# Kernel tuning notes

Measured on AMD Instinct MI355X. Metric: run time of the kernel, lower is better.

## Reference

```python
import jax, jax.numpy as jnp
import numpy as np

N0, N1, E, T = 100000, 20000, 320000, 8
D_IN, H, E_IN, C = 128, 64, 15, 16
F_LSTM = E_IN + 1  # edge feats + appended time channel


def lstm_last(x, lengths, Wih, Whh, b):
    """Unidirectional LSTM; returns hidden state at step lengths-1 per row.
    x: [E, T, F]; lengths: [E] int (1..T)."""
    Eb, Tn, _ = x.shape
    Hh = Whh.shape[0]
    xt = jnp.swapaxes(x, 0, 1)  # [T, E, F]
    h0 = jnp.zeros((Eb, Hh), x.dtype)

    def step(carry, inp):
        h, c, last_h = carry
        x_t, t = inp
        gates = x_t @ Wih + h @ Whh + b  # [E, 4H]
        i, f, g, o = jnp.split(gates, 4, axis=-1)
        c = jax.nn.sigmoid(f) * c + jax.nn.sigmoid(i) * jnp.tanh(g)
        h = jax.nn.sigmoid(o) * jnp.tanh(c)
        valid = (t < lengths)[:, None]
        last_h = jnp.where(valid, h, last_h)
        return (h, c, last_h), None

    (_, _, last_h), _ = jax.lax.scan(step, (h0, h0, h0), (xt, jnp.arange(Tn)))
    return last_h


def setup_inputs() -> dict:
    key = jax.random.key(0)
    ks = jax.random.split(key, 20)
    inp = {
        "node_features": jax.random.normal(ks[0], (N0, D_IN), jnp.float32),
        "edge_features": jax.random.normal(ks[1], (E, T, E_IN), jnp.float32),
        "seq_times": jax.random.uniform(ks[2], (E, T), jnp.float32),
        "subg_norm": jax.random.uniform(ks[3], (N1, 1), jnp.float32),
        "node_p_w": jax.random.normal(ks[4], (D_IN, 1), jnp.float32) * 0.01,
        "lstm_Wih": jax.random.normal(ks[5], (F_LSTM, 4 * H), jnp.float32) / np.sqrt(F_LSTM),
        "lstm_Whh": jax.random.normal(ks[6], (H, 4 * H), jnp.float32) / np.sqrt(H),
        "lstm_b": jnp.zeros((4 * H,), jnp.float32),
        "edge_out_W": jax.random.normal(ks[7], (D_IN + H, H), jnp.float32) / np.sqrt(D_IN + H),
        "edge_out_b": jnp.zeros((H,), jnp.float32),
        "node_W": jax.random.normal(ks[8], (D_IN + H, H), jnp.float32) / np.sqrt(D_IN + H),
        "node_b": jnp.zeros((H,), jnp.float32),
        "fc_W": jax.random.normal(ks[9], (H, C), jnp.float32) / np.sqrt(H),
        "fc_b": jnp.zeros((C,), jnp.float32),
        "edge_len": jax.random.randint(ks[10], (E,), 1, T + 1, jnp.int32),
        "src": jax.random.randint(ks[11], (E,), 0, N0, jnp.int32),
        "dst": jax.random.randint(ks[12], (E,), 0, N1, jnp.int32),
        "layer_nid": jax.random.randint(ks[13], (N1,), 0, N0, jnp.int32),
    }
    return inp


def reference(node_features, edge_features, seq_times, subg_norm, node_p_w,
              lstm_Wih, lstm_Whh, lstm_b, edge_out_W, edge_out_b,
              node_W, node_b, fc_W, fc_b,
              edge_len, src, dst, layer_nid):
    n1 = layer_nid.shape[0]
    # self features for destination nodes
    self_h = node_features[layer_nid]                         # [N1, D_IN]
    self_h_tmp = jnp.concatenate(
        [self_h, jnp.zeros((n1, H), self_h.dtype)], axis=1) @ edge_out_W + edge_out_b
    # message: gather src h, ragged LSTM over edge sequences, low-rank removal
    h_src = node_features[src]                                # [E, D_IN]
    e = jnp.concatenate([edge_features, seq_times[..., None]], axis=-1)  # [E,T,F]
    e_enc = lstm_last(e, edge_len, lstm_Wih, lstm_Whh, lstm_b)           # [E, H]
    h_proj = h_src - (h_src @ node_p_w) @ node_p_w.T          # rank-1 removal
    m = jax.nn.relu(jnp.concatenate([h_proj, e_enc], axis=1) @ edge_out_W + edge_out_b)
    # reduce: scatter-sum into destination nodes
    agg = jax.ops.segment_sum(m, dst, num_segments=n1)        # [N1, H]
    # NodeUpdate
    hu = (agg - self_h_tmp) * subg_norm
    act = jax.nn.relu(jnp.concatenate([self_h, hu], axis=1) @ node_W + node_b)
    return act @ fc_W + fc_b                                  # [N1, C]
```

## Files before the change

### kernel.cpp

```cpp
#include <hip/hip_runtime.h>

#define N0c 100000
#define N1c 20000
#define Ec 320000
#define NBLK ((Ec + 1023) / 1024)

typedef _Float16 f16;
typedef _Float16 f16x2 __attribute__((ext_vector_type(2)));

#define LOG2E 1.442695040888963f

__device__ __forceinline__ float tanh_(float x) {
    return 2.f * __builtin_amdgcn_rcpf(1.f + __builtin_amdgcn_exp2f(-2.f * LOG2E * x)) - 1.f;
}
__device__ __forceinline__ float dot2(uint w, uint v, float acc) {
#if __has_builtin(__builtin_amdgcn_fdot2)
    return __builtin_amdgcn_fdot2(__builtin_bit_cast(f16x2, w),
                                  __builtin_bit_cast(f16x2, v), acc, false);
#else
    f16x2 a = __builtin_bit_cast(f16x2, w);
    f16x2 b = __builtin_bit_cast(f16x2, v);
    return acc + (float)a[0] * (float)b[0] + (float)a[1] * (float)b[1];
#endif
}
__device__ __forceinline__ uint packh(float a, float b) {
    f16x2 p;
    p[0] = (f16)a;
    p[1] = (f16)b;
    return __builtin_bit_cast(uint, p);
}

__global__ void count_kernel(const int* __restrict__ elen, int* __restrict__ bc) {
    __shared__ int h[8];
    if (threadIdx.x < 8) h[threadIdx.x] = 0;
    __syncthreads();
    const int base = blockIdx.x * 1024;
    for (int i = threadIdx.x; i < 1024; i += 256) {
        int e = base + i;
        if (e < Ec) atomicAdd(&h[elen[e] - 1], 1);
    }
    __syncthreads();
    if (threadIdx.x < 8) bc[blockIdx.x * 8 + threadIdx.x] = h[threadIdx.x];
}

__global__ void offs_kernel(const int* __restrict__ bc, int* __restrict__ bo) {
    __shared__ int s[NBLK * 8];
    __shared__ int base[8];
    const int tid = threadIdx.x;
    for (int i = tid; i < NBLK * 8; i += 256) s[i] = bc[i];
    __syncthreads();
    if (tid == 0) {
        int tot[8];
        for (int b = 0; b < 8; ++b) {
            int t = 0;
            for (int blk = 0; blk < NBLK; ++blk) t += s[blk * 8 + b];
            tot[b] = t;
        }
        int run = 0;
        for (int b = 0; b < 8; ++b) { base[b] = run; run += tot[b]; }
    }
    __syncthreads();
    if (tid < 8) {
        int run = base[tid];
        for (int blk = 0; blk < NBLK; ++blk) {
            int t = s[blk * 8 + tid];
            s[blk * 8 + tid] = run;
            run += t;
        }
    }
    __syncthreads();
    for (int i = tid; i < NBLK * 8; i += 256) bo[i] = s[i];
}

__global__ void scatter2_kernel(const int* __restrict__ elen, const int* __restrict__ bo,
                                int* __restrict__ lperm, int* __restrict__ lenq) {
    __shared__ int cnt[256][9];
    const int tid = threadIdx.x;
    const int base = blockIdx.x * 1024 + tid * 4;
    int lens[4];
    int lc0 = 0, lc1 = 0, lc2 = 0, lc3 = 0, lc4 = 0, lc5 = 0, lc6 = 0, lc7 = 0;
    #pragma unroll
    for (int j = 0; j < 4; ++j) {
        int e = base + j;
        int l = (e < Ec) ? elen[e] - 1 : -1;
        lens[j] = l;
        lc0 += (l == 0); lc1 += (l == 1); lc2 += (l == 2); lc3 += (l == 3);
        lc4 += (l == 4); lc5 += (l == 5); lc6 += (l == 6); lc7 += (l == 7);
    }
    cnt[tid][0] = lc0; cnt[tid][1] = lc1; cnt[tid][2] = lc2; cnt[tid][3] = lc3;
    cnt[tid][4] = lc4; cnt[tid][5] = lc5; cnt[tid][6] = lc6; cnt[tid][7] = lc7;
    __syncthreads();
    if (tid < 8) {
        int run = bo[blockIdx.x * 8 + tid];
        for (int i = 0; i < 256; ++i) {
            int t = cnt[i][tid];
            cnt[i][tid] = run;
            run += t;
        }
    }
    __syncthreads();
    #pragma unroll
    for (int b = 0; b < 8; ++b) {
        int p = cnt[tid][b];
        #pragma unroll
        for (int j = 0; j < 4; ++j) {
            if (lens[j] == b) { lperm[p] = base + j; lenq[p] = b + 1; ++p; }
        }
    }
}

__global__ void dhist_kernel(const int* __restrict__ dst, int* __restrict__ hist) {
    int e = blockIdx.x * blockDim.x + threadIdx.x;
    if (e < Ec) atomicAdd(&hist[dst[e]], 1);
}

__global__ void dscan_kernel(int* __restrict__ hist) {
    __shared__ int s[N1c];
    __shared__ int psum[256];
    const int tid = threadIdx.x;
    const int CH = (N1c + 255) / 256;
    for (int i = tid; i < N1c; i += 256) s[i] = hist[i];
    __syncthreads();
    int loc = 0;
    #pragma unroll 1
    for (int j = 0; j < CH; ++j) {
        int i = tid * CH + j;
        if (i < N1c) loc += s[i];
    }
    psum[tid] = loc;
    __syncthreads();
    if (tid == 0) {
        int run = 0;
        for (int t = 0; t < 256; ++t) { int v = psum[t]; psum[t] = run; run += v; }
    }
    __syncthreads();
    int run = psum[tid];
    #pragma unroll 1
    for (int j = 0; j < CH; ++j) {
        int i = tid * CH + j;
        if (i < N1c) { int v = s[i]; s[i] = run; run += v; }
    }
    __syncthreads();
    for (int i = tid; i < N1c; i += 256) hist[i] = s[i];
}

__global__ void dscatter_kernel(const int* __restrict__ dst, int* __restrict__ cursor,
                                int* __restrict__ perm) {
    int e = blockIdx.x * blockDim.x + threadIdx.x;
    if (e < Ec) {
        int pos = atomicAdd(&cursor[dst[e]], 1);
        perm[pos] = e;
    }
}

__global__ void wprep_kernel(const float* __restrict__ Whh, const float* __restrict__ Wih,
                             const float* __restrict__ eW,
                             uint* __restrict__ wpk, uint* __restrict__ ewc) {
    int idx = blockIdx.x * 256 + threadIdx.x;
    if (idx < 40 * 256) {
        int r4 = idx >> 8, l = (idx >> 2) & 63, i = idx & 3;
        float s = (i == 2) ? (-2.f * LOG2E) : (-LOG2E);
        uint v;
        if (r4 < 32)
            v = packh(s * Whh[(2 * r4) * 256 + i * 64 + l],
                      s * Whh[(2 * r4 + 1) * 256 + i * 64 + l]);
        else {
            int kp = r4 - 32;
            v = packh(s * Wih[(2 * kp) * 256 + i * 64 + l],
                      s * Wih[(2 * kp + 1) * 256 + i * 64 + l]);
        }
        wpk[idx] = v;
    }
    if (idx < 24 * 256) {
        int c4 = idx >> 8, l = (idx >> 2) & 63, i = idx & 3;
        int cp = c4 * 4 + i;
        ewc[idx] = packh(eW[(2 * cp) * 64 + l], eW[(2 * cp + 1) * 64 + l]);
    }
}

__global__ void xprep_kernel(const float* __restrict__ ef, const float* __restrict__ st,
                             const int* __restrict__ lperm, uint* __restrict__ Xpk) {
    int idx = blockIdx.x * 256 + threadIdx.x;
    int i = idx >> 3, t = idx & 7;
    int e = lperm[i];
    float v[16];
    #pragma unroll
    for (int f = 0; f < 15; ++f) v[f] = ef[(size_t)e * 120 + t * 15 + f];
    v[15] = st[(size_t)e * 8 + t];
    uint* dst = Xpk + (size_t)idx * 8;
    #pragma unroll
    for (int j = 0; j < 8; ++j) dst[j] = packh(v[2 * j], v[2 * j + 1]);
}


__global__ __launch_bounds__(256)
void lstm4_kernel(const uint4* __restrict__ wpk4, const float* __restrict__ lb,
                  const uint* __restrict__ Xpk, const int* __restrict__ lperm,
                  const int* __restrict__ lenq, f16* __restrict__ hb)
{
    __shared__ __align__(16) uint4 sW[2560];
    __shared__ __align__(16) f16 sH[4][4 * 64];

    const int tid = threadIdx.x;
    #pragma unroll
    for (int i = 0; i < 10; ++i) sW[i * 256 + tid] = wpk4[i * 256 + tid];
    __syncthreads();

    const int lane = tid & 63;
    const int wv = tid >> 6;

    const float b0 = -LOG2E * lb[lane];
    const float b1 = -LOG2E * lb[64 + lane];
    const float b2 = -2.f * LOG2E * lb[128 + lane];
    const float b3 = -LOG2E * lb[192 + lane];
    f16* myH = sH[wv];
    const uint4* wl = sW + lane;

    const int nT = Ec / 4;
    for (int tile = blockIdx.x * 4 + wv; tile < nT; tile += gridDim.x * 4) {
        const int p0 = tile * 4;
        const int oe0 = lperm[p0], oe1 = lperm[p0 + 1], oe2 = lperm[p0 + 2], oe3 = lperm[p0 + 3];
        const int l0 = lenq[p0], l1 = lenq[p0 + 1], l2 = lenq[p0 + 2], l3 = lenq[p0 + 3];
        const int tmax = max(max(l0, l1), max(l2, l3));

        const uint* xr = Xpk + (size_t)p0 * 64;

        float hA = 0.f, cA = 0.f, hB = 0.f, cB = 0.f;
        float hC = 0.f, cC = 0.f, hD = 0.f, cD = 0.f;

        for (int t = 0; t < tmax; ++t) {
            float a0A = b0, a1A = b1, a2A = b2, a3A = b3;
            float a0B = b0, a1B = b1, a2B = b2, a3B = b3;
            float a0C = b0, a1C = b1, a2C = b2, a3C = b3;
            float a0D = b0, a1D = b1, a2D = b2, a3D = b3;

            if (t > 0) {
                #pragma unroll
                for (int jb = 0; jb < 8; ++jb) {
                    uint4 hA4 = *(const uint4*)(myH + 0 * 64 + jb * 8);
                    uint4 hB4 = *(const uint4*)(myH + 1 * 64 + jb * 8);
                    uint4 hC4 = *(const uint4*)(myH + 2 * 64 + jb * 8);
                    uint4 hD4 = *(const uint4*)(myH + 3 * 64 + jb * 8);
                    #pragma unroll
                    for (int i = 0; i < 4; ++i) {
                        uint4 w = wl[(jb * 4 + i) * 64];
                        uint hpA = (i == 0) ? hA4.x : (i == 1) ? hA4.y : (i == 2) ? hA4.z : hA4.w;
                        uint hpB = (i == 0) ? hB4.x : (i == 1) ? hB4.y : (i == 2) ? hB4.z : hB4.w;
                        uint hpC = (i == 0) ? hC4.x : (i == 1) ? hC4.y : (i == 2) ? hC4.z : hC4.w;
                        uint hpD = (i == 0) ? hD4.x : (i == 1) ? hD4.y : (i == 2) ? hD4.z : hD4.w;
                        a0A = dot2(w.x, hpA, a0A); a1A = dot2(w.y, hpA, a1A);
                        a2A = dot2(w.z, hpA, a2A); a3A = dot2(w.w, hpA, a3A);
                        a0B = dot2(w.x, hpB, a0B); a1B = dot2(w.y, hpB, a1B);
                        a2B = dot2(w.z, hpB, a2B); a3B = dot2(w.w, hpB, a3B);
                        a0C = dot2(w.x, hpC, a0C); a1C = dot2(w.y, hpC, a1C);
                        a2C = dot2(w.z, hpC, a2C); a3C = dot2(w.w, hpC, a3C);
                        a0D = dot2(w.x, hpD, a0D); a1D = dot2(w.y, hpD, a1D);
                        a2D = dot2(w.z, hpD, a2D); a3D = dot2(w.w, hpD, a3D);
                    }
                }
            }

            #pragma unroll
            for (int k4 = 0; k4 < 8; ++k4) {
                uint4 w = wl[(32 + k4) * 64];
                uint xA = xr[t * 8 + k4];
                uint xB = xr[64 + t * 8 + k4];
                uint xC = xr[128 + t * 8 + k4];
                uint xD = xr[192 + t * 8 + k4];
                a0A = dot2(w.x, xA, a0A); a1A = dot2(w.y, xA, a1A);
                a2A = dot2(w.z, xA, a2A); a3A = dot2(w.w, xA, a3A);
                a0B = dot2(w.x, xB, a0B); a1B = dot2(w.y, xB, a1B);
                a2B = dot2(w.z, xB, a2B); a3B = dot2(w.w, xB, a3B);
                a0C = dot2(w.x, xC, a0C); a1C = dot2(w.y, xC, a1C);
                a2C = dot2(w.z, xC, a2C); a3C = dot2(w.w, xC, a3C);
                a0D = dot2(w.x, xD, a0D); a1D = dot2(w.y, xD, a1D);
                a2D = dot2(w.z, xD, a2D); a3D = dot2(w.w, xD, a3D);
            }

            {
                float ig = __builtin_amdgcn_rcpf(1.f + __builtin_amdgcn_exp2f(a0A));
                float fg = __builtin_amdgcn_rcpf(1.f + __builtin_amdgcn_exp2f(a1A));
                float gg = 2.f * __builtin_amdgcn_rcpf(1.f + __builtin_amdgcn_exp2f(a2A)) - 1.f;
                float og = __builtin_amdgcn_rcpf(1.f + __builtin_amdgcn_exp2f(a3A));
                float cn = fg * cA + ig * gg, hn = og * tanh_(cn);
                if (t < l0) { cA = cn; hA = hn; }
                ig = __builtin_amdgcn_rcpf(1.f + __builtin_amdgcn_exp2f(a0B));
                fg = __builtin_amdgcn_rcpf(1.f + __builtin_amdgcn_exp2f(a1B));
                gg = 2.f * __builtin_amdgcn_rcpf(1.f + __builtin_amdgcn_exp2f(a2B)) - 1.f;
                og = __builtin_amdgcn_rcpf(1.f + __builtin_amdgcn_exp2f(a3B));
                cn = fg * cB + ig * gg; hn = og * tanh_(cn);
                if (t < l1) { cB = cn; hB = hn; }
                ig = __builtin_amdgcn_rcpf(1.f + __builtin_amdgcn_exp2f(a0C));
                fg = __builtin_amdgcn_rcpf(1.f + __builtin_amdgcn_exp2f(a1C));
                gg = 2.f * __builtin_amdgcn_rcpf(1.f + __builtin_amdgcn_exp2f(a2C)) - 1.f;
                og = __builtin_amdgcn_rcpf(1.f + __builtin_amdgcn_exp2f(a3C));
                cn = fg * cC + ig * gg; hn = og * tanh_(cn);
                if (t < l2) { cC = cn; hC = hn; }
                ig = __builtin_amdgcn_rcpf(1.f + __builtin_amdgcn_exp2f(a0D));
                fg = __builtin_amdgcn_rcpf(1.f + __builtin_amdgcn_exp2f(a1D));
                gg = 2.f * __builtin_amdgcn_rcpf(1.f + __builtin_amdgcn_exp2f(a2D)) - 1.f;
                og = __builtin_amdgcn_rcpf(1.f + __builtin_amdgcn_exp2f(a3D));
                cn = fg * cD + ig * gg; hn = og * tanh_(cn);
                if (t < l3) { cD = cn; hD = hn; }
            }
            if (t + 1 < tmax) {
                myH[0 * 64 + lane] = (f16)hA;
                myH[1 * 64 + lane] = (f16)hB;
                myH[2 * 64 + lane] = (f16)hC;
                myH[3 * 64 + lane] = (f16)hD;
            }
        }

        hb[(size_t)oe0 * 64 + lane] = (f16)hA;
        hb[(size_t)oe1 * 64 + lane] = (f16)hB;
        hb[(size_t)oe2 * 64 + lane] = (f16)hC;
        hb[(size_t)oe3 * 64 + lane] = (f16)hD;
    }
}

__global__ __launch_bounds__(256, 2)
void mlp_kernel(const float* __restrict__ nf, const float* __restrict__ pw,
                const uint4* __restrict__ ewc4, const float* __restrict__ ebias,
                const int* __restrict__ src, const f16* __restrict__ hb,
                f16* __restrict__ mbuf)
{
    __shared__ __align__(16) f16 sCat[4][192];
    const int lane = threadIdx.x & 63;
    const int wv = threadIdx.x >> 6;

    uint ew[24][4];
    #pragma unroll
    for (int i = 0; i < 24; ++i) {
        uint4 v = ewc4[i * 64 + lane];
        ew[i][0] = v.x; ew[i][1] = v.y; ew[i][2] = v.z; ew[i][3] = v.w;
    }
    const float pwl = pw[lane], pwh = pw[64 + lane];
    const float ebl = ebias[lane];

    f16* myCat = sCat[wv];
    const int wid = blockIdx.x * 4 + wv;
    const int stride = gridDim.x * 4;
    for (int e = wid; e < Ec; e += stride) {
        const int s = src[e];
        float hs0 = nf[(size_t)s * 128 + lane];
        float hs1 = nf[(size_t)s * 128 + 64 + lane];
        float part = hs0 * pwl + hs1 * pwh;
        #pragma unroll
        for (int off = 32; off; off >>= 1) part += __shfl_xor(part, off);
        float he = (float)hb[(size_t)e * 64 + lane];
        myCat[lane] = (f16)(hs0 - part * pwl);
        myCat[64 + lane] = (f16)(hs1 - part * pwh);
        myCat[128 + lane] = (f16)he;
        const uint4* cp = (const uint4*)myCat;
        float m0 = 0.f, m1 = 0.f, m2 = 0.f, m3 = 0.f;
        #pragma unroll
        for (int i = 0; i < 24; ++i) {
            uint4 q = cp[i];
            m0 = dot2(ew[i][0], q.x, m0);
            m1 = dot2(ew[i][1], q.y, m1);
            m2 = dot2(ew[i][2], q.z, m2);
            m3 = dot2(ew[i][3], q.w, m3);
        }
        float m = fmaxf(m0 + m1 + m2 + m3 + ebl, 0.f);
        mbuf[(size_t)e * 64 + lane] = (f16)m;
    }
}

#define NB_WAVES 8
#define NB_THREADS (NB_WAVES * 64)
__global__ __launch_bounds__(NB_THREADS, 1)
void node_kernel(const float* __restrict__ nf,
                 const float* __restrict__ sgn,
                 const float* __restrict__ eW,
                 const float* __restrict__ ebias,
                 const float* __restrict__ nW,
                 const float* __restrict__ nbias,
                 const float* __restrict__ fcW,
                 const float* __restrict__ fcb,
                 const int* __restrict__ lnid,
                 const int* __restrict__ hist,
                 const int* __restrict__ perm,
                 const f16* __restrict__ m,
                 float* __restrict__ out,
                 int nWavesTotal)
{
    __shared__ float sEW[128 * 64];
    __shared__ float sNW[192 * 64];
    __shared__ float sFC[64 * 16];
    __shared__ float sCat[NB_WAVES][192];
    __shared__ float sAct[NB_WAVES][64];

    const int tid = threadIdx.x;
    for (int idx = tid; idx < 128 * 64; idx += NB_THREADS) sEW[idx] = eW[idx];
    for (int idx = tid; idx < 192 * 64; idx += NB_THREADS) sNW[idx] = nW[idx];
    for (int idx = tid; idx < 64 * 16; idx += NB_THREADS) sFC[idx] = fcW[idx];
    __syncthreads();

    const int lane = tid & 63;
    const int wv = tid >> 6;
    const int gwave = blockIdx.x * NB_WAVES + wv;

    const float ebv = ebias[lane];
    const float nbv = nbias[lane];
    const float fcbv = (lane < 16) ? fcb[lane] : 0.f;

    for (int n = gwave; n < N1c; n += nWavesTotal) {
        const int nid = lnid[n];
        float sh0 = nf[(size_t)nid * 128 + lane];
        float sh1 = nf[(size_t)nid * 128 + 64 + lane];
        sCat[wv][lane] = sh0;
        sCat[wv][64 + lane] = sh1;

        float tmp = ebv;
        #pragma unroll 8
        for (int cc = 0; cc < 128; ++cc) tmp += sCat[wv][cc] * sEW[cc * 64 + lane];

        const int o0 = (n == 0) ? 0 : hist[n - 1];
        const int o1 = hist[n];
        float av = 0.f;
        for (int base = o0; base < o1; base += 64) {
            int cnt = min(64, o1 - base);
            int pk = (lane < cnt) ? perm[base + lane] : 0;
            for (int j = 0; j < cnt; ++j) {
                int pe = __shfl(pk, j);
                av += (float)m[(size_t)pe * 64 + lane];
            }
        }

        float hu = (av - tmp) * sgn[n];
        sCat[wv][128 + lane] = hu;

        float acc = nbv;
        #pragma unroll 8
        for (int cc = 0; cc < 192; ++cc) acc += sCat[wv][cc] * sNW[cc * 64 + lane];
        acc = fmaxf(acc, 0.f);
        sAct[wv][lane] = acc;

        if (lane < 16) {
            float o = fcbv;
            #pragma unroll
            for (int j = 0; j < 64; ++j) o += sAct[wv][j] * sFC[j * 16 + lane];
            out[(size_t)n * 16 + lane] = o;
        }
    }
}

extern "C" void kernel_launch(void* const* d_in, const int* in_sizes, int n_in,
                              void* d_out, int out_size, void* d_ws, size_t ws_size,
                              hipStream_t stream) {
    const float* nf  = (const float*)d_in[0];
    const float* ef  = (const float*)d_in[1];
    const float* st  = (const float*)d_in[2];
    const float* sgn = (const float*)d_in[3];
    const float* pw  = (const float*)d_in[4];
    const float* Wih = (const float*)d_in[5];
    const float* Whh = (const float*)d_in[6];
    const float* lb  = (const float*)d_in[7];
    const float* eW  = (const float*)d_in[8];
    const float* eb  = (const float*)d_in[9];
    const float* nW  = (const float*)d_in[10];
    const float* nb  = (const float*)d_in[11];
    const float* fcW = (const float*)d_in[12];
    const float* fcb = (const float*)d_in[13];
    const int* elen = (const int*)d_in[14];
    const int* src  = (const int*)d_in[15];
    const int* dst  = (const int*)d_in[16];
    const int* lnid = (const int*)d_in[17];

    float* out = (float*)d_out;

    char* base = (char*)d_ws;
    int*  hist  = (int*) (base + 0);
    int*  dperm = (int*) (base + 81920);
    int*  bc    = (int*) (base + 1392640);
    int*  bo    = (int*) (base + 1409024);
    int*  lperm = (int*) (base + 1425408);
    int*  lenq  = (int*) (base + 2736128);
    uint* wpk   = (uint*)(base + 4046848);
    uint* ewc   = (uint*)(base + 4112384);
    uint* Xpk   = (uint*)(base + 4145152);
    f16*  hb    = (f16*) (base + 86065152);
    f16*  mbuf  = (f16*) (base + 127025152);

    hipMemsetAsync(hist, 0, 81920, stream);

    count_kernel<<<NBLK, 256, 0, stream>>>(elen, bc);
    offs_kernel<<<1, 256, 0, stream>>>(bc, bo);
    scatter2_kernel<<<NBLK, 256, 0, stream>>>(elen, bo, lperm, lenq);

    dhist_kernel<<<1250, 256, 0, stream>>>(dst, hist);
    dscan_kernel<<<1, 256, 0, stream>>>(hist);
    dscatter_kernel<<<1250, 256, 0, stream>>>(dst, hist, dperm);

    wprep_kernel<<<40, 256, 0, stream>>>(Whh, Wih, eW, wpk, ewc);
    xprep_kernel<<<10000, 256, 0, stream>>>(ef, st, lperm, Xpk);

    lstm4_kernel<<<2048, 256, 0, stream>>>((const uint4*)wpk, lb, Xpk, lperm, lenq, hb);

    mlp_kernel<<<1024, 256, 0, stream>>>(nf, pw, (const uint4*)ewc, eb, src, hb, mbuf);

    node_kernel<<<512, NB_THREADS, 0, stream>>>(
        nf, sgn, eW, eb, nW, nb, fcW, fcb, lnid, hist, dperm, mbuf, out,
        512 * NB_WAVES);
}
```

Measured before the change: 866.8 us.

## Process eight edge sequences per wave in LSTM kernel with 512-thread blocks

Each wave now runs the LSTM recurrence for eight edges at once instead of four. Every LDS weight load is reused across twice as many dot products, and blocks grow to 512 threads so the shared weight copy is amortised over more waves. The cost is higher register pressure from 32 accumulators plus eight h/c pairs, which may lower occupancy. Grouping eight length-sorted edges may also add some padding work where lengths differ within a tile.

```diff
diff --git a/kernel.cpp b/kernel.cpp
--- a/kernel.cpp
+++ b/kernel.cpp
@@ -193,17 +193,17 @@
 }
 
 
-__global__ __launch_bounds__(256)
-void lstm4_kernel(const uint4* __restrict__ wpk4, const float* __restrict__ lb,
+__global__ __launch_bounds__(512)
+void lstm8_kernel(const uint4* __restrict__ wpk4, const float* __restrict__ lb,
                   const uint* __restrict__ Xpk, const int* __restrict__ lperm,
                   const int* __restrict__ lenq, f16* __restrict__ hb)
 {
     __shared__ __align__(16) uint4 sW[2560];
-    __shared__ __align__(16) f16 sH[4][4 * 64];
+    __shared__ __align__(16) f16 sH[8][8 * 64];
 
     const int tid = threadIdx.x;
     #pragma unroll
-    for (int i = 0; i < 10; ++i) sW[i * 256 + tid] = wpk4[i * 256 + tid];
+    for (int i = 0; i < 5; ++i) sW[i * 512 + tid] = wpk4[i * 512 + tid];
     __syncthreads();
 
     const int lane = tid & 63;
@@ -216,46 +216,46 @@
     f16* myH = sH[wv];
     const uint4* wl = sW + lane;
 
-    const int nT = Ec / 4;
-    for (int tile = blockIdx.x * 4 + wv; tile < nT; tile += gridDim.x * 4) {
-        const int p0 = tile * 4;
-        const int oe0 = lperm[p0], oe1 = lperm[p0 + 1], oe2 = lperm[p0 + 2], oe3 = lperm[p0 + 3];
-        const int l0 = lenq[p0], l1 = lenq[p0 + 1], l2 = lenq[p0 + 2], l3 = lenq[p0 + 3];
-        const int tmax = max(max(l0, l1), max(l2, l3));
+    const int nT = Ec / 8;
+    for (int tile = blockIdx.x * 8 + wv; tile < nT; tile += gridDim.x * 8) {
+        const int p0 = tile * 8;
+        int oe[8], ln[8];
+        #pragma unroll
+        for (int j = 0; j < 8; ++j) { oe[j] = lperm[p0 + j]; ln[j] = lenq[p0 + j]; }
+        int tmax = ln[0];
+        #pragma unroll
+        for (int j = 1; j < 8; ++j) tmax = max(tmax, ln[j]);
 
         const uint* xr = Xpk + (size_t)p0 * 64;
 
-        float hA = 0.f, cA = 0.f, hB = 0.f, cB = 0.f;
-        float hC = 0.f, cC = 0.f, hD = 0.f, cD = 0.f;
+        float h8[8], c8[8];
+        #pragma unroll
+        for (int j = 0; j < 8; ++j) { h8[j] = 0.f; c8[j] = 0.f; }
 
         for (int t = 0; t < tmax; ++t) {
-            float a0A = b0, a1A = b1, a2A = b2, a3A = b3;
-            float a0B = b0, a1B = b1, a2B = b2, a3B = b3;
-            float a0C = b0, a1C = b1, a2C = b2, a3C = b3;
-            float a0D = b0, a1D = b1, a2D = b2, a3D = b3;
+            float a0[8], a1[8], a2[8], a3[8];
+            #pragma unroll
+            for (int j = 0; j < 8; ++j) { a0[j] = b0; a1[j] = b1; a2[j] = b2; a3[j] = b3; }
 
             if (t > 0) {
                 #pragma unroll
                 for (int jb = 0; jb < 8; ++jb) {
-                    uint4 hA4 = *(const uint4*)(myH + 0 * 64 + jb * 8);
-                    uint4 hB4 = *(const uint4*)(myH + 1 * 64 + jb * 8);
-                    uint4 hC4 = *(const uint4*)(myH + 2 * 64 + jb * 8);
-                    uint4 hD4 = *(const uint4*)(myH + 3 * 64 + jb * 8);
+                    uint4 hq[8];
+                    #pragma unroll
+                    for (int j = 0; j < 8; ++j)
+                        hq[j] = *(const uint4*)(myH + j * 64 + jb * 8);
                     #pragma unroll
                     for (int i = 0; i < 4; ++i) {
                         uint4 w = wl[(jb * 4 + i) * 64];
-                        uint hpA = (i == 0) ? hA4.x : (i == 1) ? hA4.y : (i == 2) ? hA4.z : hA4.w;
-                        uint hpB = (i == 0) ? hB4.x : (i == 1) ? hB4.y : (i == 2) ? hB4.z : hB4.w;
-                        uint hpC = (i == 0) ? hC4.x : (i == 1) ? hC4.y : (i == 2) ? hC4.z : hC4.w;
-                        uint hpD = (i == 0) ? hD4.x : (i == 1) ? hD4.y : (i == 2) ? hD4.z : hD4.w;
-                        a0A = dot2(w.x, hpA, a0A); a1A = dot2(w.y, hpA, a1A);
-                        a2A = dot2(w.z, hpA, a2A); a3A = dot2(w.w, hpA, a3A);
-                        a0B = dot2(w.x, hpB, a0B); a1B = dot2(w.y, hpB, a1B);
-                        a2B = dot2(w.z, hpB, a2B); a3B = dot2(w.w, hpB, a3B);
-                        a0C = dot2(w.x, hpC, a0C); a1C = dot2(w.y, hpC, a1C);
-                        a2C = dot2(w.z, hpC, a2C); a3C = dot2(w.w, hpC, a3C);
-                        a0D = dot2(w.x, hpD, a0D); a1D = dot2(w.y, hpD, a1D);
-                        a2D = dot2(w.z, hpD, a2D); a3D = dot2(w.w, hpD, a3D);
+                        #pragma unroll
+                        for (int j = 0; j < 8; ++j) {
+                            uint hp = (i == 0) ? hq[j].x : (i == 1) ? hq[j].y
+                                    : (i == 2) ? hq[j].z : hq[j].w;
+                            a0[j] = dot2(w.x, hp, a0[j]);
+                            a1[j] = dot2(w.y, hp, a1[j]);
+                            a2[j] = dot2(w.z, hp, a2[j]);
+                            a3[j] = dot2(w.w, hp, a3[j]);
+                        }
                     }
                 }
             }
@@ -263,58 +263,35 @@
             #pragma unroll
             for (int k4 = 0; k4 < 8; ++k4) {
                 uint4 w = wl[(32 + k4) * 64];
-                uint xA = xr[t * 8 + k4];
-                uint xB = xr[64 + t * 8 + k4];
-                uint xC = xr[128 + t * 8 + k4];
-                uint xD = xr[192 + t * 8 + k4];
-                a0A = dot2(w.x, xA, a0A); a1A = dot2(w.y, xA, a1A);
-                a2A = dot2(w.z, xA, a2A); a3A = dot2(w.w, xA, a3A);
-                a0B = dot2(w.x, xB, a0B); a1B = dot2(w.y, xB, a1B);
-                a2B = dot2(w.z, xB, a2B); a3B = dot2(w.w, xB, a3B);
-                a0C = dot2(w.x, xC, a0C); a1C = dot2(w.y, xC, a1C);
-                a2C = dot2(w.z, xC, a2C); a3C = dot2(w.w, xC, a3C);
-                a0D = dot2(w.x, xD, a0D); a1D = dot2(w.y, xD, a1D);
-                a2D = dot2(w.z, xD, a2D); a3D = dot2(w.w, xD, a3D);
+                #pragma unroll
+                for (int j = 0; j < 8; ++j) {
+                    uint xv = xr[j * 64 + t * 8 + k4];
+                    a0[j] = dot2(w.x, xv, a0[j]);
+                    a1[j] = dot2(w.y, xv, a1[j]);
+                    a2[j] = dot2(w.z, xv, a2[j]);
+                    a3[j] = dot2(w.w, xv, a3[j]);
+                }
             }
 
-            {
-                float ig = __builtin_amdgcn_rcpf(1.f + __builtin_amdgcn_exp2f(a0A));
-                float fg = __builtin_amdgcn_rcpf(1.f + __builtin_amdgcn_exp2f(a1A));
-                float gg = 2.f * __builtin_amdgcn_rcpf(1.f + __builtin_amdgcn_exp2f(a2A)) - 1.f;
-                float og = __builtin_amdgcn_rcpf(1.f + __builtin_amdgcn_exp2f(a3A));
-                float cn = fg * cA + ig * gg, hn = og * tanh_(cn);
-                if (t < l0) { cA = cn; hA = hn; }
-                ig = __builtin_amdgcn_rcpf(1.f + __builtin_amdgcn_exp2f(a0B));
-                fg = __builtin_amdgcn_rcpf(1.f + __builtin_amdgcn_exp2f(a1B));
-                gg = 2.f * __builtin_amdgcn_rcpf(1.f + __builtin_amdgcn_exp2f(a2B)) - 1.f;
-                og = __builtin_amdgcn_rcpf(1.f + __builtin_amdgcn_exp2f(a3B));
-                cn = fg * cB + ig * gg; hn = og * tanh_(cn);
-                if (t < l1) { cB = cn; hB = hn; }
-                ig = __builtin_amdgcn_rcpf(1.f + __builtin_amdgcn_exp2f(a0C));
-                fg = __builtin_amdgcn_rcpf(1.f + __builtin_amdgcn_exp2f(a1C));
-                gg = 2.f * __builtin_amdgcn_rcpf(1.f + __builtin_amdgcn_exp2f(a2C)) - 1.f;
-                og = __builtin_amdgcn_rcpf(1.f + __builtin_amdgcn_exp2f(a3C));
-                cn = fg * cC + ig * gg; hn = og * tanh_(cn);
-                if (t < l2) { cC = cn; hC = hn; }
-                ig = __builtin_amdgcn_rcpf(1.f + __builtin_amdgcn_exp2f(a0D));
-                fg = __builtin_amdgcn_rcpf(1.f + __builtin_amdgcn_exp2f(a1D));
-                gg = 2.f * __builtin_amdgcn_rcpf(1.f + __builtin_amdgcn_exp2f(a2D)) - 1.f;
-                og = __builtin_amdgcn_rcpf(1.f + __builtin_amdgcn_exp2f(a3D));
-                cn = fg * cD + ig * gg; hn = og * tanh_(cn);
-                if (t < l3) { cD = cn; hD = hn; }
+            #pragma unroll
+            for (int j = 0; j < 8; ++j) {
+                float ig = __builtin_amdgcn_rcpf(1.f + __builtin_amdgcn_exp2f(a0[j]));
+                float fg = __builtin_amdgcn_rcpf(1.f + __builtin_amdgcn_exp2f(a1[j]));
+                float gg = 2.f * __builtin_amdgcn_rcpf(1.f + __builtin_amdgcn_exp2f(a2[j])) - 1.f;
+                float og = __builtin_amdgcn_rcpf(1.f + __builtin_amdgcn_exp2f(a3[j]));
+                float cn = fg * c8[j] + ig * gg;
+                float hn = og * tanh_(cn);
+                if (t < ln[j]) { c8[j] = cn; h8[j] = hn; }
             }
             if (t + 1 < tmax) {
-                myH[0 * 64 + lane] = (f16)hA;
-                myH[1 * 64 + lane] = (f16)hB;
-                myH[2 * 64 + lane] = (f16)hC;
-                myH[3 * 64 + lane] = (f16)hD;
+                #pragma unroll
+                for (int j = 0; j < 8; ++j) myH[j * 64 + lane] = (f16)h8[j];
             }
         }
 
-        hb[(size_t)oe0 * 64 + lane] = (f16)hA;
-        hb[(size_t)oe1 * 64 + lane] = (f16)hB;
-        hb[(size_t)oe2 * 64 + lane] = (f16)hC;
-        hb[(size_t)oe3 * 64 + lane] = (f16)hD;
+        #pragma unroll
+        for (int j = 0; j < 8; ++j)
+            hb[(size_t)oe[j] * 64 + lane] = (f16)h8[j];
     }
 }
 
@@ -495,7 +472,7 @@
     wprep_kernel<<<40, 256, 0, stream>>>(Whh, Wih, eW, wpk, ewc);
     xprep_kernel<<<10000, 256, 0, stream>>>(ef, st, lperm, Xpk);
 
-    lstm4_kernel<<<2048, 256, 0, stream>>>((const uint4*)wpk, lb, Xpk, lperm, lenq, hb);
+    lstm8_kernel<<<1250, 512, 0, stream>>>((const uint4*)wpk, lb, Xpk, lperm, lenq, hb);
 
     mlp_kernel<<<1024, 256, 0, stream>>>(nf, pw, (const uint4*)ewc, eb, src, hb, mbuf);
 
```

Result: slower. 954.9 us (+10.2%).
